# Kernel optimization log

Hardware: AMD Instinct MI355X
Metric: run time of the kernel (lower is better)

Reference implementation:

```python
import jax, jax.numpy as jnp
import numpy as np

EMBED = 1024
HEADS = 16
HDIM = EMBED // HEADS
WIN = 14
RANK = 16
ALPHA = 32
MLP = 4 * EMBED


def setup_inputs() -> dict:
    key = jax.random.key(0)
    ks = jax.random.split(key, 10)
    s = 0.02
    return {
        "x": jax.random.normal(ks[0], (2, 64, 64, EMBED), jnp.float32),
        "norm1_g": jnp.ones((EMBED,), jnp.float32),
        "norm1_b": jnp.zeros((EMBED,), jnp.float32),
        "qkv_w": jax.random.normal(ks[1], (EMBED, 3 * EMBED), jnp.float32) * s,
        "qkv_b": jnp.zeros((3 * EMBED,), jnp.float32),
        "lora_a": jax.random.normal(ks[2], (EMBED, RANK), jnp.float32) * s,
        "lora_b": jax.random.normal(ks[3], (RANK, 3 * EMBED), jnp.float32) * s,
        "rel_pos_h": jax.random.normal(ks[4], (2 * WIN - 1, HDIM), jnp.float32) * s,
        "rel_pos_w": jax.random.normal(ks[5], (2 * WIN - 1, HDIM), jnp.float32) * s,
        "proj_w": jax.random.normal(ks[6], (EMBED, EMBED), jnp.float32) * s,
        "proj_b": jnp.zeros((EMBED,), jnp.float32),
        "norm2_g": jnp.ones((EMBED,), jnp.float32),
        "norm2_b": jnp.zeros((EMBED,), jnp.float32),
        "mlp_w1": jax.random.normal(ks[7], (EMBED, MLP), jnp.float32) * s,
        "mlp_b1": jnp.zeros((MLP,), jnp.float32),
        "mlp_w2": jax.random.normal(ks[8], (MLP, EMBED), jnp.float32) * s,
        "mlp_b2": jnp.zeros((EMBED,), jnp.float32),
    }


def layer_norm(x, g, b, eps=1e-6):
    mu = jnp.mean(x, axis=-1, keepdims=True)
    var = jnp.var(x, axis=-1, keepdims=True)
    return (x - mu) * jax.lax.rsqrt(var + eps) * g + b


def window_partition(x, w):
    B, H, W, C = x.shape
    ph, pw = (w - H % w) % w, (w - W % w) % w
    x = jnp.pad(x, ((0, 0), (0, ph), (0, pw), (0, 0)))
    Hp, Wp = H + ph, W + pw
    x = x.reshape(B, Hp // w, w, Wp // w, w, C)
    x = x.transpose(0, 1, 3, 2, 4, 5).reshape(-1, w, w, C)
    return x, (Hp, Wp)


def window_unpartition(x, w, pad_hw, hw):
    Hp, Wp = pad_hw
    H, W = hw
    B = x.shape[0] // (Hp // w * (Wp // w))
    x = x.reshape(B, Hp // w, Wp // w, w, w, -1)
    x = x.transpose(0, 1, 3, 2, 4, 5).reshape(B, Hp, Wp, -1)
    return x[:, :H, :W, :]


def _rel_table(rel_pos, size):
    # square windows, no interpolation: table is (2*size-1, dim)
    idx = jnp.arange(size)[:, None] - jnp.arange(size)[None, :] + (size - 1)
    return rel_pos[idx]  # (size, size, dim)


def reference(x, norm1_g, norm1_b, qkv_w, qkv_b, lora_a, lora_b,
              rel_pos_h, rel_pos_w, proj_w, proj_b, norm2_g, norm2_b,
              mlp_w1, mlp_b1, mlp_w2, mlp_b2):
    shortcut = x
    xn = layer_norm(x, norm1_g, norm1_b)
    h, w = xn.shape[1], xn.shape[2]
    xw, pad_hw = window_partition(xn, WIN)
    Bw, H, W, C = xw.shape
    N = H * W
    xf = xw.reshape(Bw, N, C)
    # QKV with LoRA injection: qkv(x) + (x @ A @ B) * alpha/rank
    qkv = xf @ qkv_w + qkv_b + (xf @ lora_a @ lora_b) * (ALPHA / RANK)
    qkv = qkv.reshape(Bw, N, 3, HEADS, HDIM).transpose(2, 0, 3, 1, 4)  # 3,Bw,h,N,d
    q, k, v = qkv[0], qkv[1], qkv[2]
    scale = HDIM ** -0.5
    attn = jnp.einsum('bhnd,bhmd->bhnm', q * scale, k)  # (Bw,heads,N,N)
    # decomposed relative position bias
    Rh = _rel_table(rel_pos_h, H)  # (H,H,d)
    Rw = _rel_table(rel_pos_w, W)  # (W,W,d)
    rq = q.reshape(Bw, HEADS, H, W, HDIM)
    rel_h = jnp.einsum('bhxyd,xkd->bhxyk', rq, Rh)  # (Bw,heads,H,W,H)
    rel_w = jnp.einsum('bhxyd,ykd->bhxyk', rq, Rw)  # (Bw,heads,H,W,W)
    attn = (attn.reshape(Bw, HEADS, H, W, H, W)
            + rel_h[..., :, None] + rel_w[..., None, :]).reshape(Bw, HEADS, N, N)
    attn = jax.nn.softmax(attn, axis=-1)
    out = jnp.einsum('bhnm,bhmd->bhnd', attn, v)
    out = out.reshape(Bw, HEADS, H, W, HDIM).transpose(0, 2, 3, 1, 4).reshape(Bw, H, W, C)
    out = out @ proj_w + proj_b
    out = window_unpartition(out, WIN, pad_hw, (h, w))
    x = shortcut + out
    # MLP with exact GELU (torch default)
    xn2 = layer_norm(x, norm2_g, norm2_b)
    hmid = jax.nn.gelu(xn2 @ mlp_w1 + mlp_b1, approximate=False)
    x = x + (hmid @ mlp_w2 + mlp_b2)
    return x
```

## Files before the change

### kernel.cpp

```cpp
#include <hip/hip_runtime.h>
#include <cstdint>
#include <cstddef>


typedef __bf16 bf16x8 __attribute__((ext_vector_type(8)));
typedef float f32x4 __attribute__((ext_vector_type(4)));

__device__ __forceinline__ unsigned short f2bf(float f) {
    unsigned u = __float_as_uint(f);
    u = (u + 0x7fffu + ((u >> 16) & 1u)) >> 16;
    return (unsigned short)u;
}
__device__ __forceinline__ float bf2f(unsigned short h) {
    return __uint_as_float(((unsigned)h) << 16);
}

#define GLDS16(gp, lp) __builtin_amdgcn_global_load_lds( \
    (__attribute__((address_space(1))) unsigned int*)(gp), \
    (__attribute__((address_space(3))) unsigned int*)(lp), 16, 0, 0)

__global__ __launch_bounds__(256) void weff_kernel(
    const float* __restrict__ W, const float* __restrict__ la,
    const float* __restrict__ lb, unsigned short* __restrict__ Wt)
{
    __shared__ float tile[32][33];
    __shared__ float lat[32][16];
    __shared__ float lbt[16][32];
    const int kb = blockIdx.x * 32, nb = blockIdx.y * 32;
    const int tn = threadIdx.x & 31, tk = threadIdx.x >> 5;
    for (int i = threadIdx.x; i < 32 * 16; i += 256)
        lat[i >> 4][i & 15] = la[(size_t)(kb + (i >> 4)) * 16 + (i & 15)];
    for (int i = threadIdx.x; i < 16 * 32; i += 256)
        lbt[i >> 5][i & 31] = lb[(size_t)(i >> 5) * 3072 + nb + (i & 31)];
#pragma unroll
    for (int i = 0; i < 4; ++i) {
        int k = tk + i * 8;
        tile[k][tn] = W[(size_t)(kb + k) * 3072 + nb + tn];
    }
    __syncthreads();
#pragma unroll
    for (int i = 0; i < 4; ++i) {
        int n = tk + i * 8;
        float acc = tile[tn][n];
#pragma unroll
        for (int r = 0; r < 16; ++r) acc += 2.0f * lat[tn][r] * lbt[r][n];
        Wt[(size_t)(nb + n) * 1024 + kb + tn] = f2bf(acc);
    }
}

__global__ __launch_bounds__(256) void transpose3_kernel(
    const float* __restrict__ Wp, unsigned short* __restrict__ WpT,
    const float* __restrict__ W1, unsigned short* __restrict__ W1T,
    const float* __restrict__ W2, unsigned short* __restrict__ W2T)
{
    __shared__ float tile[32][33];
    const int id = blockIdx.x;
    const float* W; unsigned short* Wt; int Kdim, Ndim, kb, nb;
    if (id < 1024)      { W = Wp; Wt = WpT; Kdim = 1024; Ndim = 1024; const int t = id;        kb = t >> 5; nb = t & 31; }
    else if (id < 5120) { W = W1; Wt = W1T; Kdim = 1024; Ndim = 4096; const int t = id - 1024; kb = t >> 7; nb = t & 127; }
    else                { W = W2; Wt = W2T; Kdim = 4096; Ndim = 1024; const int t = id - 5120; kb = t >> 5; nb = t & 31; }
    kb <<= 5; nb <<= 5;
    const int tn = threadIdx.x & 31, tk = threadIdx.x >> 5;
#pragma unroll
    for (int i = 0; i < 4; ++i) {
        int k = tk + i * 8;
        tile[k][tn] = W[(size_t)(kb + k) * Ndim + nb + tn];
    }
    __syncthreads();
#pragma unroll
    for (int i = 0; i < 4; ++i) {
        int n = tk + i * 8;
        Wt[(size_t)(nb + n) * Kdim + kb + tn] = f2bf(tile[tn][n]);
    }
}

__global__ __launch_bounds__(256) void ln1_kernel(
    const float* __restrict__ x, const float* __restrict__ g,
    const float* __restrict__ b, unsigned short* __restrict__ out)
{
    const int blk = blockIdx.x;
    const int tid = threadIdx.x;
    const int bw = blk / 196, tok = blk - bw * 196;
    const int bat = bw / 25, rw = bw - bat * 25;
    const int wy = rw / 5, wx = rw - wy * 5;
    const int ty = tok / 14, tx = tok - ty * 14;
    const int y = wy * 14 + ty, xx = wx * 14 + tx;
    unsigned short* orow = out + (size_t)blk * 1024;
    if (y >= 64 || xx >= 64) {
        *(uint2*)(orow + tid * 4) = make_uint2(0u, 0u);
        return;
    }
    const float* irow = x + ((size_t)((bat * 64 + y) * 64 + xx)) * 1024;
    const float4 v = *(const float4*)(irow + tid * 4);
    float s = v.x + v.y + v.z + v.w;
    float ss = v.x * v.x + v.y * v.y + v.z * v.z + v.w * v.w;
    for (int o = 32; o > 0; o >>= 1) { s += __shfl_xor(s, o); ss += __shfl_xor(ss, o); }
    __shared__ float red[8];
    const int wave = tid >> 6, lane = tid & 63;
    if (lane == 0) { red[wave] = s; red[4 + wave] = ss; }
    __syncthreads();
    s = red[0] + red[1] + red[2] + red[3];
    ss = red[4] + red[5] + red[6] + red[7];
    const float mu = s * (1.0f / 1024.0f);
    const float var = ss * (1.0f / 1024.0f) - mu * mu;
    const float rstd = rsqrtf(var + 1e-6f);
    const float4 gv = *(const float4*)(g + tid * 4);
    const float4 bv = *(const float4*)(b + tid * 4);
    const float a0 = (v.x - mu) * rstd * gv.x + bv.x;
    const float a1 = (v.y - mu) * rstd * gv.y + bv.y;
    const float a2 = (v.z - mu) * rstd * gv.z + bv.z;
    const float a3 = (v.w - mu) * rstd * gv.w + bv.w;
    const unsigned r0 = (unsigned)f2bf(a0) | ((unsigned)f2bf(a1) << 16);
    const unsigned r1 = (unsigned)f2bf(a2) | ((unsigned)f2bf(a3) << 16);
    *(uint2*)(orow + tid * 4) = make_uint2(r0, r1);
}

__global__ __launch_bounds__(256) void ln2_kernel(
    const float* __restrict__ x, const float* __restrict__ g,
    const float* __restrict__ b, unsigned short* __restrict__ out)
{
    const int blk = blockIdx.x;
    const int tid = threadIdx.x;
    const float* irow = x + (size_t)blk * 1024;
    unsigned short* orow = out + (size_t)blk * 1024;
    const float4 v = *(const float4*)(irow + tid * 4);
    float s = v.x + v.y + v.z + v.w;
    float ss = v.x * v.x + v.y * v.y + v.z * v.z + v.w * v.w;
    for (int o = 32; o > 0; o >>= 1) { s += __shfl_xor(s, o); ss += __shfl_xor(ss, o); }
    __shared__ float red[8];
    const int wave = tid >> 6, lane = tid & 63;
    if (lane == 0) { red[wave] = s; red[4 + wave] = ss; }
    __syncthreads();
    s = red[0] + red[1] + red[2] + red[3];
    ss = red[4] + red[5] + red[6] + red[7];
    const float mu = s * (1.0f / 1024.0f);
    const float var = ss * (1.0f / 1024.0f) - mu * mu;
    const float rstd = rsqrtf(var + 1e-6f);
    const float4 gv = *(const float4*)(g + tid * 4);
    const float4 bv = *(const float4*)(b + tid * 4);
    const float a0 = (v.x - mu) * rstd * gv.x + bv.x;
    const float a1 = (v.y - mu) * rstd * gv.y + bv.y;
    const float a2 = (v.z - mu) * rstd * gv.z + bv.z;
    const float a3 = (v.w - mu) * rstd * gv.w + bv.w;
    const unsigned r0 = (unsigned)f2bf(a0) | ((unsigned)f2bf(a1) << 16);
    const unsigned r1 = (unsigned)f2bf(a2) | ((unsigned)f2bf(a3) << 16);
    *(uint2*)(orow + tid * 4) = make_uint2(r0, r1);
}

template <int EPI>
__global__ __launch_bounds__(512, 2) void gemm8p_v4(
    const unsigned short* __restrict__ A,
    const unsigned short* __restrict__ Bt,
    const float* __restrict__ bias,
    void* __restrict__ outp,
    int M, int K, int nbm, int nbn)
{
    __shared__ unsigned short As_s[2 * 16384];
    __shared__ unsigned short Bs_s[2 * 16384];

    const int tid = threadIdx.x;
    const int wave = tid >> 6, lane = tid & 63;
    const int lr = lane & 15, lq = lane >> 4;

    const int ss = (nbm + 7) >> 3;
    const int xcd = blockIdx.x & 7;
    const int sidx = blockIdx.x >> 3;
    const int ntl = sidx / ss;
    const int m_loc = sidx - ntl * ss;
    const int mt = xcd * ss + m_loc;
    if (mt >= nbm) return;
    const int m_base = mt * 256, n_base = ntl * 256;
    const int NT = K >> 6;

    const int wm = (wave >> 2) * 128;
    const int wn = (wave & 3) * 64;

    const int srow = tid >> 3, sslot = tid & 7;
    const int gch = sslot ^ (srow & 7);
    const unsigned short* a_gp[4];
    const unsigned short* b_gp[4];
#pragma unroll
    for (int u = 0; u < 4; ++u) {
        int ar = m_base + u * 64 + srow; ar = ar < M ? ar : M - 1;
        a_gp[u] = A + (size_t)ar * K + gch * 8;
        b_gp[u] = Bt + (size_t)(n_base + u * 64 + srow) * K + gch * 8;
    }
#define STG_A(t, u) GLDS16(a_gp[u] + (size_t)(t) * 64, As_s + (((t) & 1) << 14) + (u) * 4096 + tid * 8)
#define STG_B(t, u) GLDS16(b_gp[u] + (size_t)(t) * 64, Bs_s + (((t) & 1) << 14) + (u) * 4096 + tid * 8)

    const int sl0 = lq ^ (lr & 7);
    const int a_off = (wm + lr) * 64 + sl0 * 8;
    const int b_off = (wn + lr) * 64 + sl0 * 8;

    f32x4 acc[8][4] = {};

    STG_B(0, 0); STG_B(0, 1); STG_B(0, 2); STG_B(0, 3);
    STG_A(0, 0); STG_A(0, 2);
    STG_A(0, 1); STG_A(0, 3);
    asm volatile("s_waitcnt vmcnt(2)" ::: "memory");
    __builtin_amdgcn_s_barrier();

    for (int t = 0; t < NT; ++t) {
        const unsigned short* Ab = As_s + ((t & 1) << 14);
        const unsigned short* Bb = Bs_s + ((t & 1) << 14);
        bf16x8 af[4], bfv[4];
#pragma unroll
        for (int mf = 0; mf < 4; ++mf) af[mf] = *(const bf16x8*)(Ab + a_off + mf * 1024);
#pragma unroll
        for (int nf = 0; nf < 4; ++nf) bfv[nf] = *(const bf16x8*)(Bb + b_off + nf * 1024);
        if (t + 1 < NT) { STG_B(t + 1, 0); STG_B(t + 1, 1); }
        __builtin_amdgcn_s_barrier();
        asm volatile("s_waitcnt lgkmcnt(0)" ::: "memory");
        __builtin_amdgcn_sched_barrier(0);
        __builtin_amdgcn_s_setprio(1);
#pragma unroll
        for (int mf = 0; mf < 4; ++mf)
#pragma unroll
            for (int nf = 0; nf < 4; ++nf)
                acc[mf][nf] = __builtin_amdgcn_mfma_f32_16x16x32_bf16(af[mf], bfv[nf], acc[mf][nf], 0, 0, 0);
        __builtin_amdgcn_s_setprio(0);
        if (t == NT - 1) { asm volatile("s_waitcnt vmcnt(0)" ::: "memory"); }
        else             { asm volatile("s_waitcnt vmcnt(2)" ::: "memory"); }
        __builtin_amdgcn_s_barrier();
#pragma unroll
        for (int mf = 0; mf < 4; ++mf) af[mf] = *(const bf16x8*)(Ab + a_off + (4 + mf) * 1024);
        if (t + 1 < NT) { STG_B(t + 1, 2); STG_B(t + 1, 3); }
        __builtin_amdgcn_s_barrier();
        asm volatile("s_waitcnt lgkmcnt(0)" ::: "memory");
        __builtin_amdgcn_sched_barrier(0);
        __builtin_amdgcn_s_setprio(1);
#pragma unroll
        for (int mf = 0; mf < 4; ++mf)
#pragma unroll
            for (int nf = 0; nf < 4; ++nf)
                acc[4 + mf][nf] = __builtin_amdgcn_mfma_f32_16x16x32_bf16(af[mf], bfv[nf], acc[4 + mf][nf], 0, 0, 0);
        __builtin_amdgcn_s_setprio(0);
        __builtin_amdgcn_s_barrier();
#pragma unroll
        for (int mf = 0; mf < 4; ++mf) af[mf] = *(const bf16x8*)(Ab + (a_off ^ 32) + mf * 1024);
#pragma unroll
        for (int nf = 0; nf < 4; ++nf) bfv[nf] = *(const bf16x8*)(Bb + (b_off ^ 32) + nf * 1024);
        if (t + 1 < NT) { STG_A(t + 1, 0); STG_A(t + 1, 2); }
        __builtin_amdgcn_s_barrier();
        asm volatile("s_waitcnt lgkmcnt(0)" ::: "memory");
        __builtin_amdgcn_sched_barrier(0);
        __builtin_amdgcn_s_setprio(1);
#pragma unroll
        for (int mf = 0; mf < 4; ++mf)
#pragma unroll
            for (int nf = 0; nf < 4; ++nf)
                acc[mf][nf] = __builtin_amdgcn_mfma_f32_16x16x32_bf16(af[mf], bfv[nf], acc[mf][nf], 0, 0, 0);
        __builtin_amdgcn_s_setprio(0);
        __builtin_amdgcn_s_barrier();
#pragma unroll
        for (int mf = 0; mf < 4; ++mf) af[mf] = *(const bf16x8*)(Ab + (a_off ^ 32) + (4 + mf) * 1024);
        if (t + 1 < NT) { STG_A(t + 1, 1); STG_A(t + 1, 3); }
        __builtin_amdgcn_s_barrier();
        asm volatile("s_waitcnt lgkmcnt(0)" ::: "memory");
        __builtin_amdgcn_sched_barrier(0);
        __builtin_amdgcn_s_setprio(1);
#pragma unroll
        for (int mf = 0; mf < 4; ++mf)
#pragma unroll
            for (int nf = 0; nf < 4; ++nf)
                acc[4 + mf][nf] = __builtin_amdgcn_mfma_f32_16x16x32_bf16(af[mf], bfv[nf], acc[4 + mf][nf], 0, 0, 0);
        __builtin_amdgcn_s_setprio(0);
        if (t < NT - 1) { asm volatile("s_waitcnt vmcnt(2)" ::: "memory"); }
        __builtin_amdgcn_s_barrier();
    }
#undef STG_A
#undef STG_B

    float biasv[4];
#pragma unroll
    for (int j = 0; j < 4; ++j) biasv[j] = bias[n_base + wn + j * 16 + lr];

    if constexpr (EPI == 0) {
#pragma unroll
        for (int i = 0; i < 8; ++i) {
            const int m0i = m_base + wm + i * 16 + lq * 4;
            if (m0i >= M) continue;
            const int bw = m0i / 196, tok0 = m0i - bw * 196;
#pragma unroll
            for (int j = 0; j < 4; ++j) {
                const int n = n_base + wn + j * 16 + lr;
                const int which = n >> 10, hh = (n >> 6) & 15, d = n & 63;
                unsigned short* slotp = (unsigned short*)outp + (size_t)((bw * 3 + which) * 16 + hh) * 13312;
                if (which == 2) {
                    unsigned long long pv = 0;
#pragma unroll
                    for (int r = 0; r < 4; ++r)
                        pv |= (unsigned long long)f2bf(acc[i][j][r] + biasv[j]) << (16 * r);
                    *(unsigned long long*)(slotp + (size_t)d * 208 + tok0) = pv;
                } else {
#pragma unroll
                    for (int r = 0; r < 4; ++r)
                        slotp[(size_t)(tok0 + r) * 64 + d] = f2bf(acc[i][j][r] + biasv[j]);
                }
            }
        }
    } else {
#pragma unroll
        for (int i = 0; i < 8; ++i) {
#pragma unroll
            for (int r = 0; r < 4; ++r) {
                const int m = m_base + wm + i * 16 + lq * 4 + r;
                if (m >= M) continue;
#pragma unroll
                for (int j = 0; j < 4; ++j) {
                    const int n = n_base + wn + j * 16 + lr;
                    const float v = acc[i][j][r] + biasv[j];
                    const float t2 = 1.5957691216f * (v + 0.044715f * v * v * v);
                    const float e = __expf(-t2);
                    const float gl = v * __builtin_amdgcn_rcpf(1.0f + e);
                    ((unsigned short*)outp)[(size_t)m * 4096 + n] = f2bf(gl);
                }
            }
        }
    }
}

template <int EPI>
__global__ __launch_bounds__(256) void gemm_kernel(
    const unsigned short* __restrict__ A,
    const unsigned short* __restrict__ Bt,
    const float* __restrict__ bias,
    void* __restrict__ outp,
    const float* __restrict__ aux,
    int M, int K, int nbm, int nbn)
{
    __shared__ unsigned short As[2][128 * 32];
    __shared__ unsigned short Bs[2][128 * 32];
    const int tid = threadIdx.x;
    const int wave = tid >> 6, lane = tid & 63;
    const int lr = lane & 15, lq = lane >> 4;
    const int ss = (nbm + 7) >> 3;
    const int xcd = blockIdx.x & 7;
    const int s = blockIdx.x >> 3;
    const int nt = s / ss;
    const int m_loc = s - nt * ss;
    const int mt = xcd * ss + m_loc;
    if (mt >= nbm) return;
    const int m_base = mt * 128, n_base = nt * 128;
    const int wm = (wave >> 1) * 64, wn = (wave & 1) * 64;
    const int N = nbn * 128;

    const int c0 = tid, c1 = tid + 256;
    const int row0 = c0 >> 2, row1 = c1 >> 2;
    const int kc = (tid & 3) ^ ((tid >> 3) & 3);
    int ar0 = m_base + row0; ar0 = ar0 < M ? ar0 : M - 1;
    int ar1 = m_base + row1; ar1 = ar1 < M ? ar1 : M - 1;
    int br0 = n_base + row0; br0 = br0 < N ? br0 : N - 1;
    int br1 = n_base + row1; br1 = br1 < N ? br1 : N - 1;
    const unsigned short* agp0 = A + (size_t)ar0 * K + kc * 8;
    const unsigned short* agp1 = A + (size_t)ar1 * K + kc * 8;
    const unsigned short* bgp0 = Bt + (size_t)br0 * K + kc * 8;
    const unsigned short* bgp1 = Bt + (size_t)br1 * K + kc * 8;
    unsigned short* alp0 = As[0] + c0 * 8;
    unsigned short* alp1 = As[0] + c1 * 8;
    unsigned short* blp0 = Bs[0] + c0 * 8;
    unsigned short* blp1 = Bs[0] + c1 * 8;
    unsigned short* alp0b = As[1] + c0 * 8;
    unsigned short* alp1b = As[1] + c1 * 8;
    unsigned short* blp0b = Bs[1] + c0 * 8;
    unsigned short* blp1b = Bs[1] + c1 * 8;

    const int swz = (lq ^ ((lr >> 1) & 3)) * 8;

    f32x4 acc[4][4] = {};

    for (int k0 = 0; k0 < K; k0 += 64) {
        GLDS16(agp0 + k0, alp0);
        GLDS16(agp1 + k0, alp1);
        GLDS16(bgp0 + k0, blp0);
        GLDS16(bgp1 + k0, blp1);
        GLDS16(agp0 + k0 + 32, alp0b);
        GLDS16(agp1 + k0 + 32, alp1b);
        GLDS16(bgp0 + k0 + 32, blp0b);
        GLDS16(bgp1 + k0 + 32, blp1b);
        __syncthreads();
#pragma unroll
        for (int half = 0; half < 2; ++half) {
            bf16x8 af[4], bfr[4];
#pragma unroll
            for (int i = 0; i < 4; ++i) {
                af[i]  = *(const bf16x8*)(As[half] + (wm + i * 16 + lr) * 32 + swz);
                bfr[i] = *(const bf16x8*)(Bs[half] + (wn + i * 16 + lr) * 32 + swz);
            }
#pragma unroll
            for (int i = 0; i < 4; ++i)
#pragma unroll
                for (int j = 0; j < 4; ++j)
                    acc[i][j] = __builtin_amdgcn_mfma_f32_16x16x32_bf16(af[i], bfr[j], acc[i][j], 0, 0, 0);
        }
        __syncthreads();
    }

    float biasv[4];
#pragma unroll
    for (int j = 0; j < 4; ++j) biasv[j] = bias[n_base + wn + j * 16 + lr];

#pragma unroll
    for (int i = 0; i < 4; ++i) {
#pragma unroll
        for (int r = 0; r < 4; ++r) {
            const int m = m_base + wm + i * 16 + lq * 4 + r;
            if (m >= M) continue;
            int y = 0, xx = 0, b = 0;
            if constexpr (EPI == 1) {
                const int bw = m / 196, tok = m - bw * 196;
                b = bw / 25;
                const int rw = bw - b * 25;
                const int wy = rw / 5, wx = rw - wy * 5;
                const int ty = tok / 14, tx = tok - ty * 14;
                y = wy * 14 + ty; xx = wx * 14 + tx;
            }
#pragma unroll
            for (int j = 0; j < 4; ++j) {
                const int n = n_base + wn + j * 16 + lr;
                const float v = acc[i][j][r] + biasv[j];
                if constexpr (EPI == 1) {
                    if (y < 64 && xx < 64) {
                        const size_t idx = ((size_t)((b * 64 + y) * 64 + xx)) * 1024 + n;
                        ((float*)outp)[idx] = aux[idx] + v;
                    }
                } else {
                    const size_t idx = (size_t)m * 1024 + n;
                    ((float*)outp)[idx] += v;
                }
            }
        }
    }
}

__global__ __launch_bounds__(256, 2) void attn_kernel(
    const unsigned short* __restrict__ qkv,
    const float* __restrict__ relh, const float* __restrict__ relw,
    unsigned short* __restrict__ attn_out)
{
    __shared__ unsigned short Vt[64][232];
    __shared__ unsigned short Pst[4][16][232];
    __shared__ unsigned short Db[196][28];

    const int tid = threadIdx.x;
    const int wave = tid >> 6, lane = tid & 63;
    const int lr = lane & 15, lq = lane >> 4;
    const int bw = blockIdx.x >> 4, h = blockIdx.x & 15;
    const unsigned short* qp = qkv + (size_t)((bw * 3 + 0) * 16 + h) * 13312;
    const unsigned short* kp = qkv + (size_t)((bw * 3 + 1) * 16 + h) * 13312;
    const unsigned short* vp = qkv + (size_t)((bw * 3 + 2) * 16 + h) * 13312;

    *(uint2*)&Pst[wave][lane >> 2][208 + (lane & 3) * 4] = make_uint2(0u, 0u);

    {
        unsigned short* vtf = &Vt[0][0];
        for (int idx = tid; idx < 64 * 29; idx += 256) {
            const int d = idx / 29, c = idx - d * 29;
            GLDS16(vp + d * 208 + c * 8, vtf + idx * 8);
        }
    }

    for (int t = wave; t < 28; t += 4) {
        const int isw = t >= 14;
        const int c = isw ? t - 14 : t;
        const int arow = isw ? (lr * 14 + c) : (c * 14 + lr);
        const unsigned short* ap = qp + arow * 64 + lq * 8;
        const bf16x8 a0 = *(const bf16x8*)ap;
        const bf16x8 a1 = *(const bf16x8*)(ap + 32);
        int ridx = c - lr + 13;
        ridx = ridx < 0 ? 0 : (ridx > 26 ? 26 : ridx);
        const float* tb = (isw ? relw : relh) + ridx * 64 + lq * 8;
        union BV { unsigned short u[8]; bf16x8 v; } b0, b1;
        {
            const float4 x0 = *(const float4*)tb;
            const float4 x1 = *(const float4*)(tb + 4);
            b0.u[0] = f2bf(x0.x); b0.u[1] = f2bf(x0.y); b0.u[2] = f2bf(x0.z); b0.u[3] = f2bf(x0.w);
            b0.u[4] = f2bf(x1.x); b0.u[5] = f2bf(x1.y); b0.u[6] = f2bf(x1.z); b0.u[7] = f2bf(x1.w);
            const float4 x2 = *(const float4*)(tb + 32);
            const float4 x3 = *(const float4*)(tb + 36);
            b1.u[0] = f2bf(x2.x); b1.u[1] = f2bf(x2.y); b1.u[2] = f2bf(x2.z); b1.u[3] = f2bf(x2.w);
            b1.u[4] = f2bf(x3.x); b1.u[5] = f2bf(x3.y); b1.u[6] = f2bf(x3.z); b1.u[7] = f2bf(x3.w);
        }
        f32x4 dacc = {};
        dacc = __builtin_amdgcn_mfma_f32_16x16x32_bf16(a0, b0.v, dacc, 0, 0, 0);
        dacc = __builtin_amdgcn_mfma_f32_16x16x32_bf16(a1, b1.v, dacc, 0, 0, 0);
#pragma unroll
        for (int r = 0; r < 4; ++r) {
            const int y = lq * 4 + r;
            if (y < 14 && lr < 14) {
                const int g = isw ? y * 14 + c : c * 14 + y;
                Db[g][isw ? 14 + lr : lr] = f2bf(dacc[r]);
            }
        }
    }
    __syncthreads();

    for (int mt = wave; mt < 13; mt += 4) {
        const int m0 = mt * 16;
        const unsigned short* qb = qp + (size_t)(m0 + lr) * 64 + lq * 8;
        const bf16x8 qa0 = *(const bf16x8*)qb;
        const bf16x8 qa1 = *(const bf16x8*)(qb + 32);
        f32x4 sc[13];
#pragma unroll
        for (int nt = 0; nt < 13; ++nt) {
            const unsigned short* kb = kp + (size_t)(nt * 16 + lr) * 64 + lq * 8;
            const bf16x8 k0 = *(const bf16x8*)kb;
            const bf16x8 k1 = *(const bf16x8*)(kb + 32);
            f32x4 a = {};
            a = __builtin_amdgcn_mfma_f32_16x16x32_bf16(qa0, k0, a, 0, 0, 0);
            a = __builtin_amdgcn_mfma_f32_16x16x32_bf16(qa1, k1, a, 0, 0, 0);
            sc[nt] = a;
        }
        int grow[4];
#pragma unroll
        for (int r = 0; r < 4; ++r) {
            int g = m0 + lq * 4 + r;
            grow[r] = g > 195 ? 195 : g;
        }
#pragma unroll
        for (int nt = 0; nt < 13; ++nt) {
            const int n = nt * 16 + lr;
            if (n < 196) {
                const int nx = n / 14, ny = n - nx * 14;
#pragma unroll
                for (int r = 0; r < 4; ++r)
                    sc[nt][r] = sc[nt][r] * 0.125f + bf2f(Db[grow[r]][nx]) + bf2f(Db[grow[r]][14 + ny]);
            } else {
#pragma unroll
                for (int r = 0; r < 4; ++r) sc[nt][r] = -1e30f;
            }
        }
        float rs[4];
#pragma unroll
        for (int r = 0; r < 4; ++r) {
            float mx = sc[0][r];
#pragma unroll
            for (int nt = 1; nt < 13; ++nt) mx = fmaxf(mx, sc[nt][r]);
            mx = fmaxf(mx, __shfl_xor(mx, 1));
            mx = fmaxf(mx, __shfl_xor(mx, 2));
            mx = fmaxf(mx, __shfl_xor(mx, 4));
            mx = fmaxf(mx, __shfl_xor(mx, 8));
            float s = 0.f;
#pragma unroll
            for (int nt = 0; nt < 13; ++nt) {
                const float e = __expf(sc[nt][r] - mx);
                sc[nt][r] = e;
                s += e;
            }
            s += __shfl_xor(s, 1);
            s += __shfl_xor(s, 2);
            s += __shfl_xor(s, 4);
            s += __shfl_xor(s, 8);
            rs[r] = 1.0f / s;
        }
#pragma unroll
        for (int nt = 0; nt < 13; ++nt)
#pragma unroll
            for (int r = 0; r < 4; ++r)
                Pst[wave][lq * 4 + r][nt * 16 + lr] = f2bf(sc[nt][r]);
#pragma unroll
        for (int dt = 0; dt < 4; ++dt) {
            f32x4 a = {};
#pragma unroll
            for (int ks = 0; ks < 7; ++ks) {
                const bf16x8 pa = *(const bf16x8*)&Pst[wave][lr][ks * 32 + lq * 8];
                const bf16x8 vb = *(const bf16x8*)&Vt[dt * 16 + lr][ks * 32 + lq * 8];
                a = __builtin_amdgcn_mfma_f32_16x16x32_bf16(pa, vb, a, 0, 0, 0);
            }
#pragma unroll
            for (int r = 0; r < 4; ++r) {
                const int m = m0 + lq * 4 + r;
                if (m < 196)
                    attn_out[(size_t)(bw * 196 + m) * 1024 + h * 64 + dt * 16 + lr] = f2bf(a[r] * rs[r]);
            }
        }
    }
}

extern "C" void kernel_launch(void* const* d_in, const int* in_sizes, int n_in,
                              void* d_out, int out_size, void* d_ws, size_t ws_size,
                              hipStream_t stream)
{
    (void)in_sizes; (void)n_in; (void)out_size; (void)ws_size;
    const float* x      = (const float*)d_in[0];
    const float* n1g    = (const float*)d_in[1];
    const float* n1b    = (const float*)d_in[2];
    const float* qkv_w  = (const float*)d_in[3];
    const float* qkv_b  = (const float*)d_in[4];
    const float* lora_a = (const float*)d_in[5];
    const float* lora_b = (const float*)d_in[6];
    const float* relh   = (const float*)d_in[7];
    const float* relw   = (const float*)d_in[8];
    const float* proj_w = (const float*)d_in[9];
    const float* proj_b = (const float*)d_in[10];
    const float* n2g    = (const float*)d_in[11];
    const float* n2b    = (const float*)d_in[12];
    const float* w1     = (const float*)d_in[13];
    const float* b1     = (const float*)d_in[14];
    const float* w2     = (const float*)d_in[15];
    const float* b2     = (const float*)d_in[16];
    float* out = (float*)d_out;

    char* ws = (char*)d_ws;
    size_t off = 0;
    auto alloc = [&](size_t bytes) {
        char* p = ws + off;
        off += (bytes + 255) & ~(size_t)255;
        return p;
    };
    unsigned short* weffT = (unsigned short*)alloc((size_t)3072 * 1024 * 2);
    unsigned short* projT = (unsigned short*)alloc((size_t)1024 * 1024 * 2);
    unsigned short* w1T   = (unsigned short*)alloc((size_t)4096 * 1024 * 2);
    unsigned short* w2T   = (unsigned short*)alloc((size_t)1024 * 4096 * 2);
    unsigned short* xnw   = (unsigned short*)alloc((size_t)9800 * 1024 * 2);
    unsigned short* qkvb  = (unsigned short*)alloc((size_t)8192 * 4096 * 2);
    unsigned short* attno = (unsigned short*)alloc((size_t)9800 * 1024 * 2);

    weff_kernel<<<dim3(32, 96), 256, 0, stream>>>(qkv_w, lora_a, lora_b, weffT);
    transpose3_kernel<<<9216, 256, 0, stream>>>(proj_w, projT, w1, w1T, w2, w2T);
    ln1_kernel<<<9800, 256, 0, stream>>>(x, n1g, n1b, xnw);
    gemm8p_v4<0><<<dim3(8 * 5 * 12), 512, 0, stream>>>(xnw, weffT, qkv_b, qkvb, 9800, 1024, 39, 12);
    attn_kernel<<<800, 256, 0, stream>>>(qkvb, relh, relw, attno);
    gemm_kernel<1><<<dim3(8 * 10 * 8), 256, 0, stream>>>(attno, projT, proj_b, out, x, 9800, 1024, 77, 8);
    unsigned short* xn2 = xnw;
    ln2_kernel<<<8192, 256, 0, stream>>>(out, n2g, n2b, xn2);
    unsigned short* hmid = qkvb;
    gemm8p_v4<2><<<dim3(8 * 4 * 16), 512, 0, stream>>>(xn2, w1T, b1, hmid, 8192, 1024, 32, 16);
    gemm_kernel<3><<<dim3(8 * 8 * 8), 256, 0, stream>>>(hmid, w2T, b2, out, nullptr, 8192, 4096, 64, 8);
}
```

Baseline: 544.3 us.

## Double-buffer LDS tiles in proj and MLP-down GEMMs to overlap loads with MFMA

The proj and MLP2 GEMMs now keep two LDS stages and prefetch the next K tile with global_load_lds before computing the current one. A partial vmcnt wait replaces the full wait, so global latency can overlap matrix math. This doubles LDS use to 64KB per block, which may reduce occupancy. The synchronisation now relies on a hand-written waitcnt plus raw barriers.

```diff
diff --git a/kernel.cpp b/kernel.cpp
--- a/kernel.cpp
+++ b/kernel.cpp
@@ -321,16 +321,16 @@
 }
 
 template <int EPI>
-__global__ __launch_bounds__(256) void gemm_kernel(
+__global__ __launch_bounds__(256) void gemm_db_kernel(
     const unsigned short* __restrict__ A,
     const unsigned short* __restrict__ Bt,
     const float* __restrict__ bias,
-    void* __restrict__ outp,
+    float* __restrict__ outp,
     const float* __restrict__ aux,
     int M, int K, int nbm, int nbn)
 {
-    __shared__ unsigned short As[2][128 * 32];
-    __shared__ unsigned short Bs[2][128 * 32];
+    __shared__ unsigned short As[2][2][128 * 32];
+    __shared__ unsigned short Bs[2][2][128 * 32];
     const int tid = threadIdx.x;
     const int wave = tid >> 6, lane = tid & 63;
     const int lr = lane & 15, lq = lane >> 4;
@@ -356,36 +356,42 @@
     const unsigned short* agp1 = A + (size_t)ar1 * K + kc * 8;
     const unsigned short* bgp0 = Bt + (size_t)br0 * K + kc * 8;
     const unsigned short* bgp1 = Bt + (size_t)br1 * K + kc * 8;
-    unsigned short* alp0 = As[0] + c0 * 8;
-    unsigned short* alp1 = As[0] + c1 * 8;
-    unsigned short* blp0 = Bs[0] + c0 * 8;
-    unsigned short* blp1 = Bs[0] + c1 * 8;
-    unsigned short* alp0b = As[1] + c0 * 8;
-    unsigned short* alp1b = As[1] + c1 * 8;
-    unsigned short* blp0b = Bs[1] + c0 * 8;
-    unsigned short* blp1b = Bs[1] + c1 * 8;
+
+#define STAGE_DB(tt) do { \
+        const int _par = (tt) & 1; \
+        const size_t _ko = (size_t)(tt) * 64; \
+        GLDS16(agp0 + _ko,      As[_par][0] + c0 * 8); \
+        GLDS16(agp1 + _ko,      As[_par][0] + c1 * 8); \
+        GLDS16(bgp0 + _ko,      Bs[_par][0] + c0 * 8); \
+        GLDS16(bgp1 + _ko,      Bs[_par][0] + c1 * 8); \
+        GLDS16(agp0 + _ko + 32, As[_par][1] + c0 * 8); \
+        GLDS16(agp1 + _ko + 32, As[_par][1] + c1 * 8); \
+        GLDS16(bgp0 + _ko + 32, Bs[_par][1] + c0 * 8); \
+        GLDS16(bgp1 + _ko + 32, Bs[_par][1] + c1 * 8); \
+    } while (0)
 
     const int swz = (lq ^ ((lr >> 1) & 3)) * 8;
 
     f32x4 acc[4][4] = {};
-
-    for (int k0 = 0; k0 < K; k0 += 64) {
-        GLDS16(agp0 + k0, alp0);
-        GLDS16(agp1 + k0, alp1);
-        GLDS16(bgp0 + k0, blp0);
-        GLDS16(bgp1 + k0, blp1);
-        GLDS16(agp0 + k0 + 32, alp0b);
-        GLDS16(agp1 + k0 + 32, alp1b);
-        GLDS16(bgp0 + k0 + 32, blp0b);
-        GLDS16(bgp1 + k0 + 32, blp1b);
-        __syncthreads();
+    const int NT = K >> 6;
+
+    STAGE_DB(0);
+    for (int t = 0; t < NT; ++t) {
+        if (t + 1 < NT) {
+            STAGE_DB(t + 1);
+            asm volatile("s_waitcnt vmcnt(8)" ::: "memory");
+        } else {
+            asm volatile("s_waitcnt vmcnt(0)" ::: "memory");
+        }
+        __builtin_amdgcn_s_barrier();
+        const int par = t & 1;
 #pragma unroll
         for (int half = 0; half < 2; ++half) {
             bf16x8 af[4], bfr[4];
 #pragma unroll
             for (int i = 0; i < 4; ++i) {
-                af[i]  = *(const bf16x8*)(As[half] + (wm + i * 16 + lr) * 32 + swz);
-                bfr[i] = *(const bf16x8*)(Bs[half] + (wn + i * 16 + lr) * 32 + swz);
+                af[i]  = *(const bf16x8*)(As[par][half] + (wm + i * 16 + lr) * 32 + swz);
+                bfr[i] = *(const bf16x8*)(Bs[par][half] + (wn + i * 16 + lr) * 32 + swz);
             }
 #pragma unroll
             for (int i = 0; i < 4; ++i)
@@ -393,8 +399,9 @@
                 for (int j = 0; j < 4; ++j)
                     acc[i][j] = __builtin_amdgcn_mfma_f32_16x16x32_bf16(af[i], bfr[j], acc[i][j], 0, 0, 0);
         }
-        __syncthreads();
-    }
+        __builtin_amdgcn_s_barrier();
+    }
+#undef STAGE_DB
 
     float biasv[4];
 #pragma unroll
@@ -422,11 +429,10 @@
                 if constexpr (EPI == 1) {
                     if (y < 64 && xx < 64) {
                         const size_t idx = ((size_t)((b * 64 + y) * 64 + xx)) * 1024 + n;
-                        ((float*)outp)[idx] = aux[idx] + v;
+                        outp[idx] = aux[idx] + v;
                     }
                 } else {
-                    const size_t idx = (size_t)m * 1024 + n;
-                    ((float*)outp)[idx] += v;
+                    outp[(size_t)m * 1024 + n] += v;
                 }
             }
         }
@@ -621,10 +627,10 @@
     ln1_kernel<<<9800, 256, 0, stream>>>(x, n1g, n1b, xnw);
     gemm8p_v4<0><<<dim3(8 * 5 * 12), 512, 0, stream>>>(xnw, weffT, qkv_b, qkvb, 9800, 1024, 39, 12);
     attn_kernel<<<800, 256, 0, stream>>>(qkvb, relh, relw, attno);
-    gemm_kernel<1><<<dim3(8 * 10 * 8), 256, 0, stream>>>(attno, projT, proj_b, out, x, 9800, 1024, 77, 8);
+    gemm_db_kernel<1><<<dim3(8 * 10 * 8), 256, 0, stream>>>(attno, projT, proj_b, out, x, 9800, 1024, 77, 8);
     unsigned short* xn2 = xnw;
     ln2_kernel<<<8192, 256, 0, stream>>>(out, n2g, n2b, xn2);
     unsigned short* hmid = qkvb;
     gemm8p_v4<2><<<dim3(8 * 4 * 16), 512, 0, stream>>>(xn2, w1T, b1, hmid, 8192, 1024, 32, 16);
-    gemm_kernel<3><<<dim3(8 * 8 * 8), 256, 0, stream>>>(hmid, w2T, b2, out, nullptr, 8192, 4096, 64, 8);
-}
+    gemm_db_kernel<3><<<dim3(8 * 8 * 8), 256, 0, stream>>>(hmid, w2T, b2, out, nullptr, 8192, 4096, 64, 8);
+}
```

New measurement: 568.5 us. 4.4% more time.
